# Optimization experiments

Hardware: AMD Instinct MI355X
Metric: run time of the kernel (lower is better)

## Reference

```python
import jax, jax.numpy as jnp
import numpy as np

B, T, F, E = 256, 100, 34, 1024


def setup_inputs() -> dict:
    key = jax.random.key(0)
    ks = jax.random.split(key, 12)
    sc = 1.0 / np.sqrt(E)
    u = lambda k, shape: jax.random.uniform(k, shape, jnp.float32, -sc, sc)
    return {
        "x": jax.random.normal(ks[0], (B, T, F), jnp.float32),
        "W_lin": u(ks[1], (E, F)),
        "b_lin": u(ks[2], (E,)),
        "W_ih1": u(ks[3], (4 * E, E)),
        "W_hh1": u(ks[4], (4 * E, E)),
        "b_ih1": u(ks[5], (4 * E,)),
        "b_hh1": u(ks[6], (4 * E,)),
        "W_ih2": u(ks[7], (4 * E, E)),
        "W_hh2": u(ks[8], (4 * E, E)),
        "b_ih2": u(ks[9], (4 * E,)),
        "b_hh2": u(ks[10], (4 * E,)),
    }


def _gate_update(gates, c):
    # torch LSTMCell gate order: input, forget, cell(g), output
    i, f, g, o = jnp.split(gates, 4, axis=-1)
    c_new = jax.nn.sigmoid(f) * c + jax.nn.sigmoid(i) * jnp.tanh(g)
    h_new = jax.nn.sigmoid(o) * jnp.tanh(c_new)
    return h_new, c_new


def reference(x, W_lin, b_lin, W_ih1, W_hh1, b_ih1, b_hh1, W_ih2, W_hh2, b_ih2, b_hh2):
    hd = W_hh1.shape[1]
    bsz = x.shape[0]
    enc = x @ W_lin.T + b_lin                      # [B,T,E]
    # Precompute layer-1 input projections (incl. both biases) for all timesteps
    xg1 = jnp.einsum('bte,ge->btg', enc, W_ih1) + (b_ih1 + b_hh1)  # [B,T,4E]
    xs = jnp.swapaxes(xg1, 0, 1)                   # [T,B,4E] time-major for scan
    b2 = b_ih2 + b_hh2
    z = jnp.zeros((bsz, hd), jnp.float32)

    def step(carry, xg):
        h1, c1, h2, c2 = carry
        h1, c1 = _gate_update(xg + h1 @ W_hh1.T, c1)
        h2, c2 = _gate_update(h1 @ W_ih2.T + b2 + h2 @ W_hh2.T, c2)
        return (h1, c1, h2, c2), None

    (h1, c1, h2, c2), _ = jax.lax.scan(step, (z, z, z, z), xs)
    return (h2, c2)
```

## Files before the change

### kernel.cpp

```cpp
#include <hip/hip_runtime.h>

#define USH unsigned short
#define AGENT __HIP_MEMORY_SCOPE_AGENT
typedef __attribute__((ext_vector_type(8))) short short8;
typedef __attribute__((ext_vector_type(4))) float f32x4;

__device__ __forceinline__ USH rne_bf16(float f){
  unsigned int u = __float_as_uint(f);
  u = (u + 0x7fffu + ((u >> 16) & 1u)) >> 16;
  return (USH)u;
}
__device__ __forceinline__ float sigm(float x){ return 1.f / (1.f + __expf(-x)); }
__device__ __forceinline__ float tanh_(float x){ return 1.f - 2.f / (__expf(2.f * x) + 1.f); }
__device__ __forceinline__ void gload16(const void* g, void* l){
  __builtin_amdgcn_global_load_lds((const __attribute__((address_space(1))) unsigned int*)g,
                                   (__attribute__((address_space(3))) unsigned int*)l, 16, 0, 0);
}
__device__ __forceinline__ void st_bf16_sc1(USH* p, USH v){
  asm volatile("global_store_short %0, %1, off sc1" :: "v"(p), "v"((unsigned int)v) : "memory");
}
#define MFMA __builtin_amdgcn_mfma_f32_16x16x32_bf16

__global__ void k_fold(const float* __restrict__ Wih1, const float* __restrict__ Wlin,
                       const float* __restrict__ blin, const float* __restrict__ bih1,
                       const float* __restrict__ bhh1, USH* __restrict__ Wcpk, float* __restrict__ bc){
  const int n = blockIdx.x;
  const int t = threadIdx.x;
  float a[34];
#pragma unroll
  for (int f = 0; f < 34; ++f) a[f] = 0.f;
  float ab = 0.f;
  for (int e = t; e < 1024; e += 64){
    const float wv = Wih1[n * 1024 + e];
    ab += wv * blin[e];
    const float* wl = Wlin + e * 34;
#pragma unroll
    for (int f = 0; f < 34; ++f) a[f] += wv * wl[f];
  }
#pragma unroll
  for (int off = 32; off > 0; off >>= 1){
    ab += __shfl_down(ab, off);
#pragma unroll
    for (int f = 0; f < 34; ++f) a[f] += __shfl_down(a[f], off);
  }
  if (t == 0){
    const int nc = n & 1023, gq = n >> 10, cgi = nc >> 4, lp = nc & 15;
    for (int f = 0; f < 64; ++f){
      const float v = (f < 34) ? a[f] : 0.f;
      const int lane = lp + (((f >> 3) & 3) << 4);
      const int idx = (((cgi * 2 + (f >> 5)) * 4 + gq) * 64 + lane) * 8 + (f & 7);
      Wcpk[idx] = rne_bf16(v);
    }
    bc[n] = ab + bih1[n] + bhh1[n];
  }
}

__global__ void k_pack(const float* __restrict__ Whh1, const float* __restrict__ Wih2,
                       const float* __restrict__ Whh2, const float* __restrict__ bih2,
                       const float* __restrict__ bhh2,
                       USH* __restrict__ P1, USH* __restrict__ P2a, USH* __restrict__ P2b,
                       float* __restrict__ ob2){
  const int N = 4096 * 1024;
  for (int i = blockIdx.x * blockDim.x + threadIdx.x; i < N; i += gridDim.x * blockDim.x){
    const int j = i & 7, li = (i >> 3) & 63, gq = (i >> 9) & 3, ks = (i >> 11) & 31, cgi = i >> 16;
    const int n = gq * 1024 + cgi * 16 + (li & 15);
    const int k = ks * 32 + ((li >> 4) << 3) + j;
    const int src = n * 1024 + k;
    P1[i]  = rne_bf16(Whh1[src]);
    P2a[i] = rne_bf16(Wih2[src]);
    P2b[i] = rne_bf16(Whh2[src]);
    if (i < 4096) ob2[i] = bih2[i] + bhh2[i];
  }
}

__global__ void k_xpk(const float* __restrict__ x, USH* __restrict__ xp){
  const int N = 100 * 16384;
  for (int i = blockIdx.x * blockDim.x + threadIdx.x; i < N; i += gridDim.x * blockDim.x){
    const int j = i & 7, li = (i >> 3) & 63, ks = (i >> 9) & 1, g = (i >> 10) & 15, t = i >> 14;
    const int row = g * 16 + (li & 15);
    const int f = ks * 32 + ((li >> 4) << 3) + j;
    xp[i] = (f < 34) ? rne_bf16(x[(row * 100 + t) * 34 + f]) : (USH)0;
  }
}

__global__ __launch_bounds__(256) void k_persist(
    USH* __restrict__ hA1, USH* __restrict__ hA2,
    int* __restrict__ ctrA, int* __restrict__ ctrB,
    const USH* __restrict__ Wpk1, const USH* __restrict__ Wpk2a, const USH* __restrict__ Wpk2b,
    const USH* __restrict__ Wcpk, const USH* __restrict__ xpk,
    const float* __restrict__ bc, const float* __restrict__ b2, float* __restrict__ out,
    int d1, int d2, int useFence)
{
  __shared__ __attribute__((aligned(16))) char lds[131072];
  const int tid = threadIdx.x, w = tid >> 6, l = tid & 63;
  const int wg = blockIdx.x;
  const int isL2 = wg >> 7;
  const int cg = (wg & 127) >> 1;
  const int mh = wg & 1;
  const int gb = mh * 8 + w * 2;
  const int col = cg * 16 + (l & 15);
  const int lofs16 = l * 16;
  const int lofs8 = l * 8;

  const int ks2 = cg >> 1;
  const int l16 = (cg * 2 + ((l & 15) >> 3)) & 3;
  const int j2 = l & 7;

  float creg[2][4];
#pragma unroll
  for (int mf = 0; mf < 2; ++mf)
#pragma unroll
    for (int r = 0; r < 4; ++r) creg[mf][r] = 0.f;

  if (!isL2){
    const USH* s = Wpk1 + (size_t)cg * 65536;
#pragma unroll
    for (int r = 0; r < 32; ++r)
      gload16(s + (r * 4 + w) * 512 + lofs8, &lds[(r * 4 + w) * 1024]);
    short8 wc[2][4];
#pragma unroll
    for (int ks = 0; ks < 2; ++ks)
#pragma unroll
      for (int gq = 0; gq < 4; ++gq)
        wc[ks][gq] = *(const short8*)(Wcpk + (size_t)cg * 4096 + (ks * 4 + gq) * 512 + lofs8);
    __syncthreads();
    const float bi0 = bc[col], bi1 = bc[1024 + col], bi2 = bc[2048 + col], bi3 = bc[3072 + col];

    for (int p = 0; p < 100; ++p){
      if (p >= 1){
        if (tid == 0){
          while (__hip_atomic_load(ctrA, __ATOMIC_RELAXED, AGENT) < 128 * p)
            __builtin_amdgcn_s_sleep(1);
          if (useFence){
            while (__hip_atomic_load(ctrB, __ATOMIC_RELAXED, AGENT) < 128 * (p - 2))
              __builtin_amdgcn_s_sleep(1);
            __builtin_amdgcn_fence(__ATOMIC_ACQUIRE, "agent");
          }
        }
        __syncthreads();
      }
      f32x4 acc[2][4];
#pragma unroll
      for (int mf = 0; mf < 2; ++mf)
#pragma unroll
        for (int gq = 0; gq < 4; ++gq) acc[mf][gq] = (f32x4){0.f, 0.f, 0.f, 0.f};

      if (p > 0){
        const USH* Ap = hA1 + (size_t)((p - 1) % d1) * 262144 + gb * 16384 + lofs8;
#pragma unroll
        for (int ks = 0; ks < 32; ++ks){
          short8 a0 = *(const short8*)(Ap + ks * 512);
          short8 a1 = *(const short8*)(Ap + 16384 + ks * 512);
          const char* bb = &lds[ks * 4096 + lofs16];
#pragma unroll
          for (int gq = 0; gq < 4; ++gq){
            short8 bf = *(const short8*)(bb + gq * 1024);
            acc[0][gq] = MFMA(a0, bf, acc[0][gq], 0, 0, 0);
            acc[1][gq] = MFMA(a1, bf, acc[1][gq], 0, 0, 0);
          }
        }
      }
      const USH* Xp = xpk + (size_t)p * 16384 + gb * 1024 + lofs8;
#pragma unroll
      for (int ks = 0; ks < 2; ++ks){
        short8 a0 = *(const short8*)(Xp + ks * 512);
        short8 a1 = *(const short8*)(Xp + 1024 + ks * 512);
#pragma unroll
        for (int gq = 0; gq < 4; ++gq){
          acc[0][gq] = MFMA(a0, wc[ks][gq], acc[0][gq], 0, 0, 0);
          acc[1][gq] = MFMA(a1, wc[ks][gq], acc[1][gq], 0, 0, 0);
        }
      }
      USH* hn = hA1 + (size_t)(p % d1) * 262144;
#pragma unroll
      for (int mf = 0; mf < 2; ++mf){
        const int g2 = gb + mf;
#pragma unroll
        for (int r = 0; r < 4; ++r){
          const float gi = acc[mf][0][r] + bi0;
          const float gf = acc[mf][1][r] + bi1;
          const float gg = acc[mf][2][r] + bi2;
          const float go = acc[mf][3][r] + bi3;
          const float cn = sigm(gf) * creg[mf][r] + sigm(gi) * tanh_(gg);
          creg[mf][r] = cn;
          const int lane2 = ((l >> 4) << 2) + r + (l16 << 4);
          st_bf16_sc1(&hn[(g2 * 32 + ks2) * 512 + lane2 * 8 + j2], rne_bf16(sigm(go) * tanh_(cn)));
        }
      }
      asm volatile("s_waitcnt vmcnt(0)" ::: "memory");
      __syncthreads();
      if (tid == 0){
        if (useFence) __builtin_amdgcn_fence(__ATOMIC_RELEASE, "agent");
        __hip_atomic_fetch_add(ctrA, 1, __ATOMIC_RELAXED, AGENT);
      }
    }
  } else {
    const USH* s = Wpk2b + (size_t)cg * 65536;
#pragma unroll
    for (int r = 0; r < 24; ++r)
      gload16(s + (r * 4 + w) * 512 + lofs8, &lds[(r * 4 + w) * 1024]);
    __syncthreads();
    const float bi0 = b2[col], bi1 = b2[1024 + col], bi2 = b2[2048 + col], bi3 = b2[3072 + col];
    const USH* Wsa = Wpk2a + (size_t)cg * 65536;
    const USH* Wsb = Wpk2b + (size_t)cg * 65536;

    for (int p = 1; p <= 100; ++p){
#pragma unroll
      for (int r = 0; r < 4; ++r)
        gload16(Wsa + (r * 4 + w) * 512 + lofs8, &lds[98304 + (r * 4 + w) * 1024]);
      if (tid == 0){
        while (__hip_atomic_load(ctrA, __ATOMIC_RELAXED, AGENT) < 128 * p)
          __builtin_amdgcn_s_sleep(1);
        while (__hip_atomic_load(ctrB, __ATOMIC_RELAXED, AGENT) < 128 * (p - 1))
          __builtin_amdgcn_s_sleep(1);
        if (useFence) __builtin_amdgcn_fence(__ATOMIC_ACQUIRE, "agent");
      }
      __syncthreads();

      const USH* A1p = hA1 + (size_t)((p - 1) % d1) * 262144 + gb * 16384 + lofs8;
      const USH* A2p = hA2 + (size_t)((p - 1) % d2) * 262144 + gb * 16384 + lofs8;

      f32x4 acc[2][4];
#pragma unroll
      for (int mf = 0; mf < 2; ++mf)
#pragma unroll
        for (int gq = 0; gq < 4; ++gq) acc[mf][gq] = (f32x4){0.f, 0.f, 0.f, 0.f};

      short8 ar[2][8];
#pragma unroll
      for (int kk = 0; kk < 4; ++kk){
        ar[0][kk * 2]     = *(const short8*)(A1p + kk * 512);
        ar[0][kk * 2 + 1] = *(const short8*)(A1p + 16384 + kk * 512);
      }
#pragma unroll
      for (int c = 0; c < 10; ++c){
        if (c) __syncthreads();
        if (c < 9){
          const int t = c + 1;
          const USH* src = (t < 8) ? (Wsa + t * 8192) : (Wsb + (t - 2) * 8192);
          char* dst = &lds[98304 + (t & 1) * 16384];
#pragma unroll
          for (int r = 0; r < 4; ++r)
            gload16(src + (r * 4 + w) * 512 + lofs8, dst + (r * 4 + w) * 1024);
          const USH* Ab = (t < 8) ? A1p : A2p;
          const int ksb = (t < 8) ? t * 4 : (t - 2) * 4;
#pragma unroll
          for (int kk = 0; kk < 4; ++kk){
            ar[t & 1][kk * 2]     = *(const short8*)(Ab + (ksb + kk) * 512);
            ar[t & 1][kk * 2 + 1] = *(const short8*)(Ab + 16384 + (ksb + kk) * 512);
          }
        }
        const int rb = (c < 8) ? 2 * c : 16 + 4 * (c - 8);
        const int rn = (c < 8) ? 2 : 4;
        short8 ra[4][2];
#pragma unroll
        for (int q = 0; q < 4; ++q){
          if (q < rn){
            ra[q][0] = *(const short8*)(A2p + (rb + q) * 512);
            ra[q][1] = *(const short8*)(A2p + 16384 + (rb + q) * 512);
          }
        }
        const char* cb = &lds[98304 + (c & 1) * 16384 + lofs16];
#pragma unroll
        for (int kk = 0; kk < 4; ++kk){
#pragma unroll
          for (int gq = 0; gq < 4; ++gq){
            short8 bf = *(const short8*)(cb + kk * 4096 + gq * 1024);
            acc[0][gq] = MFMA(ar[c & 1][kk * 2],     bf, acc[0][gq], 0, 0, 0);
            acc[1][gq] = MFMA(ar[c & 1][kk * 2 + 1], bf, acc[1][gq], 0, 0, 0);
          }
        }
#pragma unroll
        for (int q = 0; q < 4; ++q){
          if (q < rn){
            const char* bb = &lds[(rb + q) * 4096 + lofs16];
#pragma unroll
            for (int gq = 0; gq < 4; ++gq){
              short8 bf = *(const short8*)(bb + gq * 1024);
              acc[0][gq] = MFMA(ra[q][0], bf, acc[0][gq], 0, 0, 0);
              acc[1][gq] = MFMA(ra[q][1], bf, acc[1][gq], 0, 0, 0);
            }
          }
        }
      }

      if (p < 100){
        USH* hn = hA2 + (size_t)(p % d2) * 262144;
#pragma unroll
        for (int mf = 0; mf < 2; ++mf){
          const int g2 = gb + mf;
#pragma unroll
          for (int r = 0; r < 4; ++r){
            const float gi = acc[mf][0][r] + bi0;
            const float gf = acc[mf][1][r] + bi1;
            const float gg = acc[mf][2][r] + bi2;
            const float go = acc[mf][3][r] + bi3;
            const float cn = sigm(gf) * creg[mf][r] + sigm(gi) * tanh_(gg);
            creg[mf][r] = cn;
            const int lane2 = ((l >> 4) << 2) + r + (l16 << 4);
            st_bf16_sc1(&hn[(g2 * 32 + ks2) * 512 + lane2 * 8 + j2], rne_bf16(sigm(go) * tanh_(cn)));
          }
        }
      } else {
#pragma unroll
        for (int mf = 0; mf < 2; ++mf){
#pragma unroll
          for (int r = 0; r < 4; ++r){
            const int row = (gb + mf) * 16 + ((l >> 4) << 2) + r;
            const float gi = acc[mf][0][r] + bi0;
            const float gf = acc[mf][1][r] + bi1;
            const float gg = acc[mf][2][r] + bi2;
            const float go = acc[mf][3][r] + bi3;
            const float cn = sigm(gf) * creg[mf][r] + sigm(gi) * tanh_(gg);
            out[row * 1024 + col] = sigm(go) * tanh_(cn);
            out[262144 + row * 1024 + col] = cn;
          }
        }
      }
      asm volatile("s_waitcnt vmcnt(0)" ::: "memory");
      __syncthreads();
      if (tid == 0){
        if (useFence) __builtin_amdgcn_fence(__ATOMIC_RELEASE, "agent");
        __hip_atomic_fetch_add(ctrB, 1, __ATOMIC_RELAXED, AGENT);
      }
    }
  }
}

extern "C" void kernel_launch(void* const* d_in, const int* in_sizes, int n_in,
                              void* d_out, int out_size, void* d_ws, size_t ws_size,
                              hipStream_t stream){
  const float* x    = (const float*)d_in[0];
  const float* Wlin = (const float*)d_in[1];
  const float* blin = (const float*)d_in[2];
  const float* Wih1 = (const float*)d_in[3];
  const float* Whh1 = (const float*)d_in[4];
  const float* bih1 = (const float*)d_in[5];
  const float* bhh1 = (const float*)d_in[6];
  const float* Wih2 = (const float*)d_in[7];
  const float* Whh2 = (const float*)d_in[8];
  const float* bih2 = (const float*)d_in[9];
  const float* bhh2 = (const float*)d_in[10];
  char* ws = (char*)d_ws;

  const size_t SLOT = 524288;
  int d1 = 100, d2 = 100, useFence = 0;
  const size_t need = 1024 + 200 * SLOT + 3 * 8388608ull + 524288 + 3276800 + 32768;
  if (ws_size < need){ d1 = 3; d2 = 2; useFence = 1; }

  size_t off = 0;
  int*   ctrA  = (int*)(ws + off);  off += 128;
  int*   ctrB  = (int*)(ws + off);  off = 1024;
  USH*   hA2   = (USH*)(ws + off);  off += (size_t)d2 * SLOT;
  USH*   hA1   = (USH*)(ws + off);  off += (size_t)d1 * SLOT;
  USH*   Wpk1  = (USH*)(ws + off);  off += 8388608;
  USH*   Wpk2a = (USH*)(ws + off);  off += 8388608;
  USH*   Wpk2b = (USH*)(ws + off);  off += 8388608;
  USH*   Wcpk  = (USH*)(ws + off);  off += 524288;
  USH*   xpk   = (USH*)(ws + off);  off += 3276800;
  float* bc    = (float*)(ws + off); off += 16384;
  float* b2    = (float*)(ws + off);

  hipMemsetAsync(ws, 0, 1024 + SLOT, stream);
  k_fold<<<4096, 64, 0, stream>>>(Wih1, Wlin, blin, bih1, bhh1, Wcpk, bc);
  k_pack<<<2048, 256, 0, stream>>>(Whh1, Wih2, Whh2, bih2, bhh2, Wpk1, Wpk2a, Wpk2b, b2);
  k_xpk<<<1024, 256, 0, stream>>>(x, xpk);

  float* outp = (float*)d_out;
  void* args[] = {&hA1, &hA2, &ctrA, &ctrB, &Wpk1, &Wpk2a, &Wpk2b, &Wcpk, &xpk, &bc, &b2, &outp,
                  &d1, &d2, &useFence};
  hipError_t e = hipLaunchCooperativeKernel((void*)k_persist, dim3(256), dim3(256), args, 0, stream);
  if (e != hipSuccess){
    k_persist<<<dim3(256), dim3(256), 0, stream>>>(hA1, hA2, ctrA, ctrB, Wpk1, Wpk2a, Wpk2b,
                                                   Wcpk, xpk, bc, b2, outp, d1, d2, useFence);
  }
}
```

Before: 1.823 ms.

## Replace shared atomic counters with per-workgroup flags polled by a full wavefront

Swaps the two global counters, which every workgroup hit with atomic fetch_add each step, for one flag word per workgroup that is written with a plain atomic store. The waiting side now uses 64 lanes, each reading four flags, and a wave vote decides when all producers are done. The goal is to remove atomic contention on a single address and shorten the spin-wait at each of the 100 timesteps. In exchange every poll reads 256 flags instead of one, and the layer-1 branch passes a target of -1 for the layer-2 flags when fencing is off.

```diff
diff --git a/kernel.cpp b/kernel.cpp
--- a/kernel.cpp
+++ b/kernel.cpp
@@ -20,6 +20,20 @@
   asm volatile("global_store_short %0, %1, off sc1" :: "v"(p), "v"((unsigned int)v) : "memory");
 }
 #define MFMA __builtin_amdgcn_mfma_f32_16x16x32_bf16
+
+__device__ __forceinline__ void waitflags(const int* f, int tA, int tB, int l){
+  const int* q = f + ((l < 32) ? (l * 4) : (128 + (l - 32) * 4));
+  const int tgt = (l < 32) ? tA : tB;
+  for (;;){
+    int v0 = __hip_atomic_load(q + 0, __ATOMIC_RELAXED, AGENT);
+    int v1 = __hip_atomic_load(q + 1, __ATOMIC_RELAXED, AGENT);
+    int v2 = __hip_atomic_load(q + 2, __ATOMIC_RELAXED, AGENT);
+    int v3 = __hip_atomic_load(q + 3, __ATOMIC_RELAXED, AGENT);
+    int m = min(min(v0, v1), min(v2, v3));
+    if (__all(m >= tgt)) return;
+    __builtin_amdgcn_s_sleep(1);
+  }
+}
 
 __global__ void k_fold(const float* __restrict__ Wih1, const float* __restrict__ Wlin,
                        const float* __restrict__ blin, const float* __restrict__ bih1,
@@ -84,8 +98,7 @@
 }
 
 __global__ __launch_bounds__(256) void k_persist(
-    USH* __restrict__ hA1, USH* __restrict__ hA2,
-    int* __restrict__ ctrA, int* __restrict__ ctrB,
+    USH* __restrict__ hA1, USH* __restrict__ hA2, int* __restrict__ flags,
     const USH* __restrict__ Wpk1, const USH* __restrict__ Wpk2a, const USH* __restrict__ Wpk2b,
     const USH* __restrict__ Wcpk, const USH* __restrict__ xpk,
     const float* __restrict__ bc, const float* __restrict__ b2, float* __restrict__ out,
@@ -128,14 +141,9 @@
 
     for (int p = 0; p < 100; ++p){
       if (p >= 1){
-        if (tid == 0){
-          while (__hip_atomic_load(ctrA, __ATOMIC_RELAXED, AGENT) < 128 * p)
-            __builtin_amdgcn_s_sleep(1);
-          if (useFence){
-            while (__hip_atomic_load(ctrB, __ATOMIC_RELAXED, AGENT) < 128 * (p - 2))
-              __builtin_amdgcn_s_sleep(1);
-            __builtin_amdgcn_fence(__ATOMIC_ACQUIRE, "agent");
-          }
+        if (tid < 64){
+          waitflags(flags, p, useFence ? (p - 2) : -1, tid);
+          if (useFence && tid == 0) __builtin_amdgcn_fence(__ATOMIC_ACQUIRE, "agent");
         }
         __syncthreads();
       }
@@ -191,7 +199,7 @@
       __syncthreads();
       if (tid == 0){
         if (useFence) __builtin_amdgcn_fence(__ATOMIC_RELEASE, "agent");
-        __hip_atomic_fetch_add(ctrA, 1, __ATOMIC_RELAXED, AGENT);
+        __hip_atomic_store(&flags[wg], p + 1, __ATOMIC_RELAXED, AGENT);
       }
     }
   } else {
@@ -208,12 +216,9 @@
 #pragma unroll
       for (int r = 0; r < 4; ++r)
         gload16(Wsa + (r * 4 + w) * 512 + lofs8, &lds[98304 + (r * 4 + w) * 1024]);
-      if (tid == 0){
-        while (__hip_atomic_load(ctrA, __ATOMIC_RELAXED, AGENT) < 128 * p)
-          __builtin_amdgcn_s_sleep(1);
-        while (__hip_atomic_load(ctrB, __ATOMIC_RELAXED, AGENT) < 128 * (p - 1))
-          __builtin_amdgcn_s_sleep(1);
-        if (useFence) __builtin_amdgcn_fence(__ATOMIC_ACQUIRE, "agent");
+      if (tid < 64){
+        waitflags(flags, p, p - 1, tid);
+        if (useFence && tid == 0) __builtin_amdgcn_fence(__ATOMIC_ACQUIRE, "agent");
       }
       __syncthreads();
 
@@ -321,7 +326,7 @@
       __syncthreads();
       if (tid == 0){
         if (useFence) __builtin_amdgcn_fence(__ATOMIC_RELEASE, "agent");
-        __hip_atomic_fetch_add(ctrB, 1, __ATOMIC_RELAXED, AGENT);
+        __hip_atomic_store(&flags[wg], p, __ATOMIC_RELAXED, AGENT);
       }
     }
   }
@@ -349,8 +354,7 @@
   if (ws_size < need){ d1 = 3; d2 = 2; useFence = 1; }
 
   size_t off = 0;
-  int*   ctrA  = (int*)(ws + off);  off += 128;
-  int*   ctrB  = (int*)(ws + off);  off = 1024;
+  int*   flags = (int*)(ws + off);  off = 1024;
   USH*   hA2   = (USH*)(ws + off);  off += (size_t)d2 * SLOT;
   USH*   hA1   = (USH*)(ws + off);  off += (size_t)d1 * SLOT;
   USH*   Wpk1  = (USH*)(ws + off);  off += 8388608;
@@ -367,11 +371,11 @@
   k_xpk<<<1024, 256, 0, stream>>>(x, xpk);
 
   float* outp = (float*)d_out;
-  void* args[] = {&hA1, &hA2, &ctrA, &ctrB, &Wpk1, &Wpk2a, &Wpk2b, &Wcpk, &xpk, &bc, &b2, &outp,
+  void* args[] = {&hA1, &hA2, &flags, &Wpk1, &Wpk2a, &Wpk2b, &Wcpk, &xpk, &bc, &b2, &outp,
                   &d1, &d2, &useFence};
   hipError_t e = hipLaunchCooperativeKernel((void*)k_persist, dim3(256), dim3(256), args, 0, stream);
   if (e != hipSuccess){
-    k_persist<<<dim3(256), dim3(256), 0, stream>>>(hA1, hA2, ctrA, ctrB, Wpk1, Wpk2a, Wpk2b,
+    k_persist<<<dim3(256), dim3(256), 0, stream>>>(hA1, hA2, flags, Wpk1, Wpk2a, Wpk2b,
                                                    Wcpk, xpk, bc, b2, outp, d1, d2, useFence);
   }
 }
```

After: 1.980 ms. 1.09x slower.
